# Optimization experiments

Measured on AMD Instinct MI355X. Metric: run time of the kernel, lower is better.

The kernel has to match this reference:

```python
import jax, jax.numpy as jnp
import numpy as np

B, C, H, W, WS, SH, NH, P = 64, 512, 28, 28, 7, 3, 16, 10
MLP_H = 2048
EPS = 1e-5
NW = (H // WS) * (W // WS)  # 16 windows per image
N = P + WS * WS             # 59 tokens per window
HEAD_D = C // NH
SCALE = HEAD_D ** -0.5


def _rel_pos_index(ws):
    coords = np.stack(np.meshgrid(np.arange(ws), np.arange(ws), indexing='ij')).reshape(2, -1)
    rel = (coords[:, :, None] - coords[:, None, :]).transpose(1, 2, 0)
    rel[..., 0] += ws - 1
    rel[..., 1] += ws - 1
    rel[..., 0] *= 2 * ws - 1
    return rel.sum(-1)  # (ws*ws, ws*ws)


def _attn_mask(h, w, ws, shift):
    img = np.zeros((h, w), dtype=np.float32)
    slices = (slice(0, -ws), slice(-ws, -shift), slice(-shift, None))
    cnt = 0
    for hs in slices:
        for wsl in slices:
            img[hs, wsl] = cnt
            cnt += 1
    mw = img.reshape(h // ws, ws, w // ws, ws).transpose(0, 2, 1, 3).reshape(-1, ws * ws)
    diff = mw[:, None, :] - mw[:, :, None]
    return np.where(diff != 0, -100.0, 0.0).astype(np.float32)  # (nW, ws*ws, ws*ws)


_RPI = jnp.asarray(_rel_pos_index(WS))
_MASK = jnp.asarray(_attn_mask(H, W, WS, SH))


def _ln(x, g, b):
    mu = jnp.mean(x, -1, keepdims=True)
    var = jnp.mean((x - mu) ** 2, -1, keepdims=True)
    return (x - mu) * jax.lax.rsqrt(var + EPS) * g + b


def _window_partition(x, ws):
    b, h, w, c = x.shape
    x = x.reshape(b, h // ws, ws, w // ws, ws, c).transpose(0, 1, 3, 2, 4, 5)
    return x.reshape(-1, ws, ws, c)


def _window_reverse(win, ws, h, w):
    b = win.shape[0] // ((h // ws) * (w // ws))
    x = win.reshape(b, h // ws, w // ws, ws, ws, -1).transpose(0, 1, 3, 2, 4, 5)
    return x.reshape(b, h, w, -1)


def setup_inputs() -> dict:
    key = jax.random.key(0)
    ks = jax.random.split(key, 8)
    d = {
        'x': jax.random.normal(ks[0], (B, P + H * W, C), jnp.float32),
        'g1': jnp.ones((C,), jnp.float32),
        'b1': jnp.zeros((C,), jnp.float32),
        'qkv_w': jax.random.normal(ks[1], (3 * C, C), jnp.float32) * 0.02,
        'qkv_b': jnp.zeros((3 * C,), jnp.float32),
        'rpb_table': jax.random.normal(ks[2], ((2 * WS - 1) ** 2, NH), jnp.float32) * 0.02,
        'proj_w': jax.random.normal(ks[3], (C, C), jnp.float32) * 0.02,
        'proj_b': jnp.zeros((C,), jnp.float32),
        'g2': jnp.ones((C,), jnp.float32),
        'b2': jnp.zeros((C,), jnp.float32),
        'fc1_w': jax.random.normal(ks[4], (MLP_H, C), jnp.float32) * 0.02,
        'fc1_b': jnp.zeros((MLP_H,), jnp.float32),
        'fc2_w': jax.random.normal(ks[5], (C, MLP_H), jnp.float32) * 0.02,
        'fc2_b': jnp.zeros((C,), jnp.float32),
    }
    return d


def _block(x, g1, b1, qkv_w, qkv_b, rpb_table, proj_w, proj_b, g2, b2, fc1_w, fc1_b, fc2_w, fc2_b):
    prompt = x[:, :P, :]                       # (B, P, C)
    x = x[:, P:, :]                            # (B, H*W, C)
    shortcut = x
    xn = _ln(x, g1, b1).reshape(B, H, W, C)
    # cyclic shift
    xn = jnp.roll(xn, shift=(-SH, -SH), axis=(1, 2))
    xw = _window_partition(xn, WS).reshape(-1, WS * WS, C)  # (B*nW, 49, C)
    # prompt padding (matches torch expand(nW,...).reshape order: index = w*B + b)
    pw = jnp.broadcast_to(prompt[None], (NW, B, P, C)).reshape(-1, P, C)
    xw = jnp.concatenate([pw, xw], axis=1)     # (B*nW, N, C)
    B_ = B * NW
    # attention
    qkv = (xw @ qkv_w.T + qkv_b).reshape(B_, N, 3, NH, HEAD_D).transpose(2, 0, 3, 1, 4)
    q, k, v = qkv[0], qkv[1], qkv[2]
    attn = jnp.einsum('bhnd,bhmd->bhnm', q * SCALE, k)  # (B_, NH, N, N)
    bias = rpb_table[_RPI.reshape(-1)].reshape(WS * WS, WS * WS, NH).transpose(2, 0, 1)
    bias = jnp.pad(bias, ((0, 0), (P, 0), (P, 0)))       # (NH, N, N)
    mask = jnp.pad(_MASK, ((0, 0), (P, 0), (P, 0)))      # (nW, N, N)
    attn = attn + bias[None]
    attn = attn.reshape(B, NW, NH, N, N) + mask[None, :, None]
    attn = jax.nn.softmax(attn.reshape(B_, NH, N, N), axis=-1)
    out = jnp.einsum('bhnm,bhmd->bhnd', attn, v).transpose(0, 2, 1, 3).reshape(B_, N, C)
    out = out @ proj_w.T + proj_b
    # drop prompts, un-window, un-shift
    out = out[:, P:, :].reshape(-1, WS, WS, C)
    xs = _window_reverse(out, WS, H, W)
    xs = jnp.roll(xs, shift=(SH, SH), axis=(1, 2)).reshape(B, H * W, C)
    x = shortcut + xs
    # MLP (exact GELU, as torch nn.GELU)
    h = _ln(x, g2, b2)
    h = jax.nn.gelu(h @ fc1_w.T + fc1_b, approximate=False)
    h = h @ fc2_w.T + fc2_b
    return x + h


def reference(x, g1, b1, qkv_w, qkv_b, rpb_table, proj_w, proj_b, g2, b2, fc1_w, fc1_b, fc2_w, fc2_b):
    return _block(x, g1, b1, qkv_w, qkv_b, rpb_table, proj_w, proj_b, g2, b2, fc1_w, fc1_b, fc2_w, fc2_b)
```

## Files before the change

kernel.cpp:

```cpp
#include <hip/hip_runtime.h>
#include <stdint.h>

typedef unsigned short u16;
typedef unsigned int u32;
typedef __attribute__((ext_vector_type(8))) short short8;
typedef __attribute__((ext_vector_type(4))) float f32x4;

__device__ __forceinline__ u16 f2bf(float f) {
  u32 u = __builtin_bit_cast(u32, f);
  u32 r = u + 0x7FFFu + ((u >> 16) & 1u);
  return (u16)(r >> 16);
}

__device__ __forceinline__ void gl_lds16(const void* g, void* l) {
  __builtin_amdgcn_global_load_lds((__attribute__((address_space(1))) void*)g,
                                   (__attribute__((address_space(3))) void*)l,
                                   16, 0, 0);
}

__global__ __launch_bounds__(256) void cvt_bf16(const float* __restrict__ in,
                                                u16* __restrict__ out, int n4) {
  int idx = blockIdx.x * 256 + threadIdx.x;
  if (idx < n4) {
    float4 v = ((const float4*)in)[idx];
    u32 lo = (u32)f2bf(v.x) | ((u32)f2bf(v.y) << 16);
    u32 hi = (u32)f2bf(v.z) | ((u32)f2bf(v.w) << 16);
    ((uint2*)out)[idx] = make_uint2(lo, hi);
  }
}

__global__ __launch_bounds__(256) void ln1_kernel(const float* __restrict__ x,
                                                  const float* __restrict__ g,
                                                  const float* __restrict__ bta,
                                                  u16* __restrict__ xcat) {
  int wave = threadIdx.x >> 6, lane = threadIdx.x & 63;
  int row = blockIdx.x * 4 + wave;
  const float* src;
  bool do_ln;
  if (row < 640) {
    int bb = row / 10, p = row - bb * 10;
    src = x + ((size_t)bb * 794 + p) * 512;
    do_ln = false;
  } else {
    int r2 = row - 640;
    int i = r2 / 49, t = r2 - i * 49;
    int bb = i >> 4, nw = i & 15;
    int tr = t / 7, tc = t - tr * 7;
    int hh = (nw >> 2) * 7 + tr + 3; if (hh >= 28) hh -= 28;
    int ww = (nw & 3) * 7 + tc + 3;  if (ww >= 28) ww -= 28;
    src = x + ((size_t)bb * 794 + 10 + hh * 28 + ww) * 512;
    do_ln = true;
  }
  float4 v0 = ((const float4*)src)[lane * 2];
  float4 v1 = ((const float4*)src)[lane * 2 + 1];
  float vals[8] = {v0.x, v0.y, v0.z, v0.w, v1.x, v1.y, v1.z, v1.w};
  u16 ob[8];
  if (do_ln) {
    float s = 0.f, s2 = 0.f;
#pragma unroll
    for (int j = 0; j < 8; ++j) { s += vals[j]; s2 += vals[j] * vals[j]; }
#pragma unroll
    for (int o = 32; o > 0; o >>= 1) { s += __shfl_xor(s, o); s2 += __shfl_xor(s2, o); }
    float mu = s * (1.0f / 512.0f);
    float var = s2 * (1.0f / 512.0f) - mu * mu;
    float inv = rsqrtf(var + 1e-5f);
    float4 ga = ((const float4*)g)[lane * 2], gb = ((const float4*)g)[lane * 2 + 1];
    float4 ba = ((const float4*)bta)[lane * 2], bb2 = ((const float4*)bta)[lane * 2 + 1];
    float gv[8] = {ga.x, ga.y, ga.z, ga.w, gb.x, gb.y, gb.z, gb.w};
    float bv[8] = {ba.x, ba.y, ba.z, ba.w, bb2.x, bb2.y, bb2.z, bb2.w};
#pragma unroll
    for (int j = 0; j < 8; ++j) ob[j] = f2bf((vals[j] - mu) * inv * gv[j] + bv[j]);
  } else {
#pragma unroll
    for (int j = 0; j < 8; ++j) ob[j] = f2bf(vals[j]);
  }
  u32 w0 = (u32)ob[0] | ((u32)ob[1] << 16);
  u32 w1 = (u32)ob[2] | ((u32)ob[3] << 16);
  u32 w2 = (u32)ob[4] | ((u32)ob[5] << 16);
  u32 w3 = (u32)ob[6] | ((u32)ob[7] << 16);
  ((uint4*)(xcat + (size_t)row * 512))[lane] = make_uint4(w0, w1, w2, w3);
}

__global__ __launch_bounds__(256) void ln2_kernel(const float* __restrict__ xn,
                                                  const float* __restrict__ g,
                                                  const float* __restrict__ bta,
                                                  u16* __restrict__ outb) {
  int wave = threadIdx.x >> 6, lane = threadIdx.x & 63;
  size_t row = (size_t)blockIdx.x * 4 + wave;
  const float* src = xn + row * 512;
  float4 v0 = ((const float4*)src)[lane * 2];
  float4 v1 = ((const float4*)src)[lane * 2 + 1];
  float vals[8] = {v0.x, v0.y, v0.z, v0.w, v1.x, v1.y, v1.z, v1.w};
  float s = 0.f, s2 = 0.f;
#pragma unroll
  for (int j = 0; j < 8; ++j) { s += vals[j]; s2 += vals[j] * vals[j]; }
#pragma unroll
  for (int o = 32; o > 0; o >>= 1) { s += __shfl_xor(s, o); s2 += __shfl_xor(s2, o); }
  float mu = s * (1.0f / 512.0f);
  float var = s2 * (1.0f / 512.0f) - mu * mu;
  float inv = rsqrtf(var + 1e-5f);
  float4 ga = ((const float4*)g)[lane * 2], gb = ((const float4*)g)[lane * 2 + 1];
  float4 ba = ((const float4*)bta)[lane * 2], bb2 = ((const float4*)bta)[lane * 2 + 1];
  float gv[8] = {ga.x, ga.y, ga.z, ga.w, gb.x, gb.y, gb.z, gb.w};
  float bv[8] = {ba.x, ba.y, ba.z, ba.w, bb2.x, bb2.y, bb2.z, bb2.w};
  u16 ob[8];
#pragma unroll
  for (int j = 0; j < 8; ++j) ob[j] = f2bf((vals[j] - mu) * inv * gv[j] + bv[j]);
  u32 w0 = (u32)ob[0] | ((u32)ob[1] << 16);
  u32 w1 = (u32)ob[2] | ((u32)ob[3] << 16);
  u32 w2 = (u32)ob[4] | ((u32)ob[5] << 16);
  u32 w3 = (u32)ob[6] | ((u32)ob[7] << 16);
  ((uint4*)(outb + row * 512))[lane] = make_uint4(w0, w1, w2, w3);
}

template <int EPI>
__global__ __launch_bounds__(256) void gemm128(const u16* __restrict__ A,
                                               const u16* __restrict__ Wt,
                                               const float* __restrict__ bias,
                                               u16* __restrict__ outb,
                                               float* __restrict__ outf,
                                               const float* __restrict__ res,
                                               int M, int N, int K) {
  __shared__ __align__(16) u16 Al[3][128 * 32];
  __shared__ __align__(16) u16 Bl[3][128 * 32];
  const int tid = threadIdx.x;
  const int lane = tid & 63;
  const int wv = tid >> 6;
  const int wm = wv >> 1, wn = wv & 1;
  const int tm = blockIdx.y * 128, tn = blockIdx.x * 128;
  const int lr = lane & 15;
  const int lk = (lane >> 4) * 8;

  f32x4 acc[4][4];
#pragma unroll
  for (int m = 0; m < 4; ++m)
#pragma unroll
    for (int n = 0; n < 4; ++n)
#pragma unroll
      for (int r2 = 0; r2 < 4; ++r2) acc[m][n][r2] = 0.f;

  const int rA = tid >> 2;
  const int kA = (tid & 3) * 8;
  const u16* Abase = A + (size_t)(tm + rA) * K + kA;
  const u16* Bbase = Wt + (size_t)(tn + rA) * K + kA;
  const size_t k64 = (size_t)64 * K;
  const int NT = K >> 5;

#define STAGE(buf, kk)                                          \
  do {                                                          \
    gl_lds16(Abase + (kk), &Al[buf][tid * 8]);                  \
    gl_lds16(Abase + k64 + (kk), &Al[buf][2048 + tid * 8]);     \
    gl_lds16(Bbase + (kk), &Bl[buf][tid * 8]);                  \
    gl_lds16(Bbase + k64 + (kk), &Bl[buf][2048 + tid * 8]);     \
  } while (0)

  STAGE(0, 0);
  STAGE(1, 32);

  int cur = 0;
  for (int t = 0; t < NT; ++t) {
    if (t < NT - 1) asm volatile("s_waitcnt vmcnt(4)" ::: "memory");
    else            asm volatile("s_waitcnt vmcnt(0)" ::: "memory");
    __builtin_amdgcn_s_barrier();
    asm volatile("" ::: "memory");

    if (t + 2 < NT) {
      int nb = cur + 2; if (nb >= 3) nb -= 3;
      STAGE(nb, (t + 2) * 32);
    }

    short8 af[4], bf[4];
#pragma unroll
    for (int m = 0; m < 4; ++m)
      af[m] = *(const short8*)&Al[cur][(wm * 64 + m * 16 + lr) * 32 + lk];
#pragma unroll
    for (int n = 0; n < 4; ++n)
      bf[n] = *(const short8*)&Bl[cur][(wn * 64 + n * 16 + lr) * 32 + lk];
#pragma unroll
    for (int m = 0; m < 4; ++m)
#pragma unroll
      for (int n = 0; n < 4; ++n)
        acc[m][n] = __builtin_amdgcn_mfma_f32_16x16x32_bf16(af[m], bf[n], acc[m][n], 0, 0, 0);

    asm volatile("" ::: "memory");
    cur = cur + 1; if (cur >= 3) cur -= 3;
  }
#undef STAGE

  float bcol[4];
#pragma unroll
  for (int n = 0; n < 4; ++n) bcol[n] = bias[tn + wn * 64 + n * 16 + lr];

#pragma unroll
  for (int m = 0; m < 4; ++m) {
#pragma unroll
    for (int r2 = 0; r2 < 4; ++r2) {
      int grow = tm + wm * 64 + m * 16 + (lane >> 4) * 4 + r2;
      if (EPI == 1) {
        int i = grow / 49, t = grow - i * 49;
        int bb = i >> 4, nw = i & 15;
        int tr = t / 7, tc = t - tr * 7;
        int hh = (nw >> 2) * 7 + tr + 3; if (hh >= 28) hh -= 28;
        int ww = (nw & 3) * 7 + tc + 3;  if (ww >= 28) ww -= 28;
        size_t dstr = ((size_t)bb * 784 + hh * 28 + ww) * 512;
        size_t srcr = ((size_t)bb * 794 + 10 + hh * 28 + ww) * 512;
#pragma unroll
        for (int n = 0; n < 4; ++n) {
          int gcol = tn + wn * 64 + n * 16 + lr;
          float v = acc[m][n][r2] + bcol[n];
          outf[dstr + gcol] = v + res[srcr + gcol];
        }
      } else {
#pragma unroll
        for (int n = 0; n < 4; ++n) {
          int gcol = tn + wn * 64 + n * 16 + lr;
          float v = acc[m][n][r2] + bcol[n];
          if (EPI == 0) {
            outb[(size_t)grow * N + gcol] = f2bf(v);
          } else if (EPI == 2) {
            float gel = 0.5f * v * (1.0f + erff(v * 0.70710678118654752f));
            outb[(size_t)grow * N + gcol] = f2bf(gel);
          } else {
            outf[(size_t)grow * N + gcol] = v + res[(size_t)grow * 512 + gcol];
          }
        }
      }
    }
  }
}

__global__ __launch_bounds__(64) void attn_kernel(const u16* __restrict__ Y,
                                                  const float* __restrict__ rpb,
                                                  u16* __restrict__ outp) {
  __shared__ __align__(16) u16 Plds[64 * 64];
  __shared__ __align__(16) u16 Vt[32 * 64];
  __shared__ float biasl[169];
  const int lane = threadIdx.x;
  const int i = blockIdx.x >> 4;
  const int hd = blockIdx.x & 15;
  const int bp = i & 63;
  const int nw = i & 15;
  const int hi = nw >> 2, wi = nw & 3;
  const int lr = lane & 15;
  const int lk = (lane >> 4) * 8;

  for (int j = lane; j < 169; j += 64) biasl[j] = rpb[j * 16 + hd];

  short8 qf[4], kf[4];
#pragma unroll
  for (int m = 0; m < 4; ++m) {
    int t = m * 16 + lr;
    size_t r = (t < 10) ? (size_t)(bp * 10 + t) : (size_t)(640 + i * 49 + (t - 10));
    const u16* base = Y + r * 1536 + hd * 32 + lk;
    if (t < 59) {
      qf[m] = *(const short8*)(base);
      kf[m] = *(const short8*)(base + 512);
    } else {
#pragma unroll
      for (int e = 0; e < 8; ++e) { qf[m][e] = 0; kf[m][e] = 0; }
    }
  }
  {
    int t = lane;
    if (t < 59) {
      size_t r = (t < 10) ? (size_t)(bp * 10 + t) : (size_t)(640 + i * 49 + (t - 10));
      const u16* vp = Y + r * 1536 + 1024 + hd * 32;
      short8 vv0 = *(const short8*)(vp);
      short8 vv1 = *(const short8*)(vp + 8);
      short8 vv2 = *(const short8*)(vp + 16);
      short8 vv3 = *(const short8*)(vp + 24);
#pragma unroll
      for (int e = 0; e < 8; ++e) {
        Vt[e * 64 + t] = (u16)vv0[e];
        Vt[(8 + e) * 64 + t] = (u16)vv1[e];
        Vt[(16 + e) * 64 + t] = (u16)vv2[e];
        Vt[(24 + e) * 64 + t] = (u16)vv3[e];
      }
    } else {
      for (int d = 0; d < 32; ++d) Vt[d * 64 + t] = 0;
    }
  }

  f32x4 s[4][4];
#pragma unroll
  for (int m = 0; m < 4; ++m)
#pragma unroll
    for (int n = 0; n < 4; ++n)
#pragma unroll
      for (int r2 = 0; r2 < 4; ++r2) s[m][n][r2] = 0.f;
#pragma unroll
  for (int m = 0; m < 4; ++m)
#pragma unroll
    for (int n = 0; n < 4; ++n)
      s[m][n] = __builtin_amdgcn_mfma_f32_16x16x32_bf16(qf[m], kf[n], s[m][n], 0, 0, 0);

  __syncthreads();

  const float SCALE = 0.17677669529663687f;
  const int rgrp = lane >> 4;
#pragma unroll
  for (int m = 0; m < 4; ++m) {
#pragma unroll
    for (int r2 = 0; r2 < 4; ++r2) {
      int rn = m * 16 + rgrp * 4 + r2;
      int qa = rn - 10;
      int qra = qa / 7, qca = qa - qra * 7;
      int regA = 0;
      if (qa >= 0 && qa < 49) {
        int ha = hi * 7 + qra, wa = wi * 7 + qca;
        regA = (ha < 21 ? 0 : (ha < 25 ? 1 : 2)) * 3 + (wa < 21 ? 0 : (wa < 25 ? 1 : 2));
      }
      float vloc[4];
      float mx = -3.0e38f;
#pragma unroll
      for (int n = 0; n < 4; ++n) {
        int cm = n * 16 + lr;
        float v;
        if (cm >= 59) {
          v = -3.0e38f;
        } else {
          v = s[m][n][r2] * SCALE;
          if (rn >= 10 && rn < 59 && cm >= 10) {
            int kb = cm - 10;
            int krb = kb / 7, kcb = kb - krb * 7;
            v += biasl[(qra - krb + 6) * 13 + (qca - kcb + 6)];
            int hb = hi * 7 + krb, wb = wi * 7 + kcb;
            int regB = (hb < 21 ? 0 : (hb < 25 ? 1 : 2)) * 3 + (wb < 21 ? 0 : (wb < 25 ? 1 : 2));
            if (regA != regB) v -= 100.0f;
          }
        }
        vloc[n] = v;
        mx = fmaxf(mx, v);
      }
#pragma unroll
      for (int o = 8; o > 0; o >>= 1) mx = fmaxf(mx, __shfl_xor(mx, o));
      float sum = 0.f;
#pragma unroll
      for (int n = 0; n < 4; ++n) {
        float e = __expf(vloc[n] - mx);
        vloc[n] = e;
        sum += e;
      }
#pragma unroll
      for (int o = 8; o > 0; o >>= 1) sum += __shfl_xor(sum, o);
      float inv = 1.0f / sum;
#pragma unroll
      for (int n = 0; n < 4; ++n)
        Plds[rn * 64 + n * 16 + lr] = f2bf(vloc[n] * inv);
    }
  }

  __syncthreads();

  f32x4 o[4][2];
#pragma unroll
  for (int m = 0; m < 4; ++m)
#pragma unroll
    for (int j = 0; j < 2; ++j)
#pragma unroll
      for (int r2 = 0; r2 < 4; ++r2) o[m][j][r2] = 0.f;
#pragma unroll
  for (int ks = 0; ks < 2; ++ks) {
    short8 pf[4], vf[2];
#pragma unroll
    for (int m = 0; m < 4; ++m)
      pf[m] = *(const short8*)&Plds[(m * 16 + lr) * 64 + ks * 32 + lk];
#pragma unroll
    for (int j = 0; j < 2; ++j)
      vf[j] = *(const short8*)&Vt[(j * 16 + lr) * 64 + ks * 32 + lk];
#pragma unroll
    for (int m = 0; m < 4; ++m)
#pragma unroll
      for (int j = 0; j < 2; ++j)
        o[m][j] = __builtin_amdgcn_mfma_f32_16x16x32_bf16(pf[m], vf[j], o[m][j], 0, 0, 0);
  }

#pragma unroll
  for (int m = 0; m < 4; ++m) {
#pragma unroll
    for (int r2 = 0; r2 < 4; ++r2) {
      int rn = m * 16 + rgrp * 4 + r2;
      if (rn >= 10 && rn < 59) {
        size_t row = (size_t)i * 49 + (rn - 10);
        u16* op = outp + row * 512 + hd * 32;
        op[lr] = f2bf(o[m][0][r2]);
        op[16 + lr] = f2bf(o[m][1][r2]);
      }
    }
  }
}

extern "C" void kernel_launch(void* const* d_in, const int* in_sizes, int n_in,
                              void* d_out, int out_size, void* d_ws, size_t ws_size,
                              hipStream_t stream) {
  const float* x = (const float*)d_in[0];
  const float* g1 = (const float*)d_in[1];
  const float* b1 = (const float*)d_in[2];
  const float* qkv_w = (const float*)d_in[3];
  const float* qkv_b = (const float*)d_in[4];
  const float* rpb = (const float*)d_in[5];
  const float* proj_w = (const float*)d_in[6];
  const float* proj_b = (const float*)d_in[7];
  const float* g2 = (const float*)d_in[8];
  const float* b2 = (const float*)d_in[9];
  const float* fc1_w = (const float*)d_in[10];
  const float* fc1_b = (const float*)d_in[11];
  const float* fc2_w = (const float*)d_in[12];
  const float* fc2_b = (const float*)d_in[13];
  float* out = (float*)d_out;

  char* ws = (char*)d_ws;
  u16* qkv_wb = (u16*)(ws + 0);
  u16* proj_wb = (u16*)(ws + 1572864);
  u16* fc1_wb = (u16*)(ws + 2097152);
  u16* fc2_wb = (u16*)(ws + 4194304);
  u16* xcat = (u16*)(ws + 6291456);
  u16* y = (u16*)(ws + 58327040);
  u16* attnv = (u16*)(ws + 214433792);
  float* xnew = (float*)(ws + 265814016);
  u16* hin = xcat;
  u16* hmid = y;

  cvt_bf16<<<768, 256, 0, stream>>>(qkv_w, qkv_wb, 196608);
  cvt_bf16<<<256, 256, 0, stream>>>(proj_w, proj_wb, 65536);
  cvt_bf16<<<1024, 256, 0, stream>>>(fc1_w, fc1_wb, 262144);
  cvt_bf16<<<1024, 256, 0, stream>>>(fc2_w, fc2_wb, 262144);

  ln1_kernel<<<12704, 256, 0, stream>>>(x, g1, b1, xcat);

  gemm128<0><<<dim3(12, 397), 256, 0, stream>>>(xcat, qkv_wb, qkv_b, y, nullptr, nullptr,
                                                50816, 1536, 512);

  attn_kernel<<<16384, 64, 0, stream>>>(y, rpb, attnv);

  gemm128<1><<<dim3(4, 392), 256, 0, stream>>>(attnv, proj_wb, proj_b, nullptr, xnew, x,
                                               50176, 512, 512);

  ln2_kernel<<<12544, 256, 0, stream>>>(xnew, g2, b2, hin);

  gemm128<2><<<dim3(16, 392), 256, 0, stream>>>(hin, fc1_wb, fc1_b, hmid, nullptr, nullptr,
                                                50176, 2048, 512);

  gemm128<3><<<dim3(4, 392), 256, 0, stream>>>(hmid, fc2_wb, fc2_b, nullptr, out, xnew,
                                               50176, 512, 2048);
}
```

Before: 763.5 us.

## Replace 128x128 GEMM with 256x256 tiled, swizzled, XCD-remapped GEMM kernel

The GEMM kernel moves from 128x128 tiles with BK=32 and a triple buffer to 256x256 tiles with BK=64 and a double buffer, run by 512 threads over a 1D grid. Shared-memory rows use an XOR swizzle to avoid bank conflicts, and block indices are remapped so each XCD handles a contiguous range of tiles, which should help L2 reuse. MFMA issue is wrapped in s_setprio, and the epilogue now guards rows past M. The larger tiles raise arithmetic intensity per load but use about 128KB of LDS per block, which likely limits occupancy to one block per CU and leaves a partial last M tile for the QKV GEMM.

After: 821.9 us. +7.6%, slower.

```diff
diff --git a/kernel.cpp b/kernel.cpp
--- a/kernel.cpp
+++ b/kernel.cpp
@@ -114,76 +114,100 @@
 }
 
 template <int EPI>
-__global__ __launch_bounds__(256) void gemm128(const u16* __restrict__ A,
-                                               const u16* __restrict__ Wt,
-                                               const float* __restrict__ bias,
-                                               u16* __restrict__ outb,
-                                               float* __restrict__ outf,
-                                               const float* __restrict__ res,
-                                               int M, int N, int K) {
-  __shared__ __align__(16) u16 Al[3][128 * 32];
-  __shared__ __align__(16) u16 Bl[3][128 * 32];
+__global__ __launch_bounds__(512, 2) void gemm256(const u16* __restrict__ A,
+                                                  const u16* __restrict__ Wt,
+                                                  const float* __restrict__ bias,
+                                                  u16* __restrict__ outb,
+                                                  float* __restrict__ outf,
+                                                  const float* __restrict__ res,
+                                                  int M, int N, int K, int Ntiles) {
+  __shared__ __align__(16) u16 Al[2][256 * 64];
+  __shared__ __align__(16) u16 Bl[2][256 * 64];
   const int tid = threadIdx.x;
   const int lane = tid & 63;
   const int wv = tid >> 6;
-  const int wm = wv >> 1, wn = wv & 1;
-  const int tm = blockIdx.y * 128, tn = blockIdx.x * 128;
+  const int wm = wv >> 2, wn = wv & 3;
   const int lr = lane & 15;
-  const int lk = (lane >> 4) * 8;
-
-  f32x4 acc[4][4];
-#pragma unroll
-  for (int m = 0; m < 4; ++m)
+  const int qh = lane >> 4;
+
+  const int nwg = gridDim.x;
+  const int qx = nwg >> 3, rx = nwg & 7;
+  const int xcd = blockIdx.x & 7, local = blockIdx.x >> 3;
+  const int swz = (xcd < rx ? xcd * (qx + 1) : rx * (qx + 1) + (xcd - rx) * qx) + local;
+  const int mt = swz / Ntiles, nt = swz - mt * Ntiles;
+  const int tm = mt * 256, tn = nt * 256;
+
+  f32x4 acc[8][4];
+#pragma unroll
+  for (int m = 0; m < 8; ++m)
 #pragma unroll
     for (int n = 0; n < 4; ++n)
 #pragma unroll
-      for (int r2 = 0; r2 < 4; ++r2) acc[m][n][r2] = 0.f;
-
-  const int rA = tid >> 2;
-  const int kA = (tid & 3) * 8;
-  const u16* Abase = A + (size_t)(tm + rA) * K + kA;
-  const u16* Bbase = Wt + (size_t)(tn + rA) * K + kA;
-  const size_t k64 = (size_t)64 * K;
-  const int NT = K >> 5;
-
-#define STAGE(buf, kk)                                          \
-  do {                                                          \
-    gl_lds16(Abase + (kk), &Al[buf][tid * 8]);                  \
-    gl_lds16(Abase + k64 + (kk), &Al[buf][2048 + tid * 8]);     \
-    gl_lds16(Bbase + (kk), &Bl[buf][tid * 8]);                  \
-    gl_lds16(Bbase + k64 + (kk), &Bl[buf][2048 + tid * 8]);     \
+      for (int e = 0; e < 4; ++e) acc[m][n][e] = 0.f;
+
+  const int slot = tid & 7;
+  const int r0 = tid >> 3;
+  const int scol = ((slot ^ (r0 & 7)) << 3);
+  const u16* Ap0 = A + (size_t)(tm + r0) * K + scol;
+  const u16* Ap1 = A + (size_t)(tm + r0 + 64) * K + scol;
+  const u16* Ap2 = A + (size_t)(tm + r0 + 128) * K + scol;
+  const u16* Ap3 = A + (size_t)(tm + r0 + 192) * K + scol;
+  const u16* Bp0 = Wt + (size_t)(tn + r0) * K + scol;
+  const u16* Bp1 = Wt + (size_t)(tn + r0 + 64) * K + scol;
+  const u16* Bp2 = Wt + (size_t)(tn + r0 + 128) * K + scol;
+  const u16* Bp3 = Wt + (size_t)(tn + r0 + 192) * K + scol;
+
+#define STAGE(buf, k0)                                      \
+  do {                                                      \
+    u16* al = &Al[buf][tid * 8];                            \
+    u16* bl = &Bl[buf][tid * 8];                            \
+    gl_lds16(Ap0 + (k0), al);                               \
+    gl_lds16(Ap1 + (k0), al + 4096);                        \
+    gl_lds16(Ap2 + (k0), al + 8192);                        \
+    gl_lds16(Ap3 + (k0), al + 12288);                       \
+    gl_lds16(Bp0 + (k0), bl);                               \
+    gl_lds16(Bp1 + (k0), bl + 4096);                        \
+    gl_lds16(Bp2 + (k0), bl + 8192);                        \
+    gl_lds16(Bp3 + (k0), bl + 12288);                       \
   } while (0)
 
+  const int NT = K >> 6;
   STAGE(0, 0);
-  STAGE(1, 32);
-
-  int cur = 0;
+
   for (int t = 0; t < NT; ++t) {
-    if (t < NT - 1) asm volatile("s_waitcnt vmcnt(4)" ::: "memory");
-    else            asm volatile("s_waitcnt vmcnt(0)" ::: "memory");
+    const int cur = t & 1;
+    if (t + 1 < NT) {
+      __builtin_amdgcn_s_barrier();
+      asm volatile("" ::: "memory");
+      STAGE(cur ^ 1, (t + 1) << 6);
+      asm volatile("s_waitcnt vmcnt(8)" ::: "memory");
+    } else {
+      asm volatile("s_waitcnt vmcnt(0)" ::: "memory");
+    }
     __builtin_amdgcn_s_barrier();
     asm volatile("" ::: "memory");
 
-    if (t + 2 < NT) {
-      int nb = cur + 2; if (nb >= 3) nb -= 3;
-      STAGE(nb, (t + 2) * 32);
-    }
-
-    short8 af[4], bf[4];
-#pragma unroll
-    for (int m = 0; m < 4; ++m)
-      af[m] = *(const short8*)&Al[cur][(wm * 64 + m * 16 + lr) * 32 + lk];
-#pragma unroll
-    for (int n = 0; n < 4; ++n)
-      bf[n] = *(const short8*)&Bl[cur][(wn * 64 + n * 16 + lr) * 32 + lk];
-#pragma unroll
-    for (int m = 0; m < 4; ++m)
+    const u16* Ab = &Al[cur][0];
+    const u16* Bb = &Bl[cur][0];
+#pragma unroll
+    for (int ks = 0; ks < 2; ++ks) {
+      const int sw = (((ks << 2) | qh) ^ (lr & 7)) << 3;
+      short8 av[8], bv[4];
+#pragma unroll
+      for (int m = 0; m < 8; ++m)
+        av[m] = *(const short8*)&Ab[(wm * 128 + m * 16 + lr) * 64 + sw];
 #pragma unroll
       for (int n = 0; n < 4; ++n)
-        acc[m][n] = __builtin_amdgcn_mfma_f32_16x16x32_bf16(af[m], bf[n], acc[m][n], 0, 0, 0);
-
+        bv[n] = *(const short8*)&Bb[(wn * 64 + n * 16 + lr) * 64 + sw];
+      __builtin_amdgcn_s_setprio(1);
+#pragma unroll
+      for (int m = 0; m < 8; ++m)
+#pragma unroll
+        for (int n = 0; n < 4; ++n)
+          acc[m][n] = __builtin_amdgcn_mfma_f32_16x16x32_bf16(av[m], bv[n], acc[m][n], 0, 0, 0);
+      __builtin_amdgcn_s_setprio(0);
+    }
     asm volatile("" ::: "memory");
-    cur = cur + 1; if (cur >= 3) cur -= 3;
   }
 #undef STAGE
 
@@ -192,10 +216,11 @@
   for (int n = 0; n < 4; ++n) bcol[n] = bias[tn + wn * 64 + n * 16 + lr];
 
 #pragma unroll
-  for (int m = 0; m < 4; ++m) {
+  for (int m = 0; m < 8; ++m) {
 #pragma unroll
     for (int r2 = 0; r2 < 4; ++r2) {
-      int grow = tm + wm * 64 + m * 16 + (lane >> 4) * 4 + r2;
+      int grow = tm + wm * 128 + m * 16 + qh * 4 + r2;
+      if (grow >= M) continue;
       if (EPI == 1) {
         int i = grow / 49, t = grow - i * 49;
         int bb = i >> 4, nw = i & 15;
@@ -428,19 +453,19 @@
 
   ln1_kernel<<<12704, 256, 0, stream>>>(x, g1, b1, xcat);
 
-  gemm128<0><<<dim3(12, 397), 256, 0, stream>>>(xcat, qkv_wb, qkv_b, y, nullptr, nullptr,
-                                                50816, 1536, 512);
+  gemm256<0><<<199 * 6, 512, 0, stream>>>(xcat, qkv_wb, qkv_b, y, nullptr, nullptr,
+                                          50816, 1536, 512, 6);
 
   attn_kernel<<<16384, 64, 0, stream>>>(y, rpb, attnv);
 
-  gemm128<1><<<dim3(4, 392), 256, 0, stream>>>(attnv, proj_wb, proj_b, nullptr, xnew, x,
-                                               50176, 512, 512);
+  gemm256<1><<<196 * 2, 512, 0, stream>>>(attnv, proj_wb, proj_b, nullptr, xnew, x,
+                                          50176, 512, 512, 2);
 
   ln2_kernel<<<12544, 256, 0, stream>>>(xnew, g2, b2, hin);
 
-  gemm128<2><<<dim3(16, 392), 256, 0, stream>>>(hin, fc1_wb, fc1_b, hmid, nullptr, nullptr,
-                                                50176, 2048, 512);
-
-  gemm128<3><<<dim3(4, 392), 256, 0, stream>>>(hmid, fc2_wb, fc2_b, nullptr, out, xnew,
-                                               50176, 512, 2048);
-}
+  gemm256<2><<<196 * 8, 512, 0, stream>>>(hin, fc1_wb, fc1_b, hmid, nullptr, nullptr,
+                                          50176, 2048, 512, 8);
+
+  gemm256<3><<<196 * 2, 512, 0, stream>>>(hmid, fc2_wb, fc2_b, nullptr, out, xnew,
+                                          50176, 512, 2048, 2);
+}
```
